# Optimization experiments

Measured on AMD Instinct MI355X. Metric: run time of the kernel, lower is better.

## Reference

```python
import jax, jax.numpy as jnp
import numpy as np

D_MODEL = 1024
NUM_HEADS = 16
HEAD_SIZE = D_MODEL // NUM_HEADS
ROPE_BASE = 10000.0
RMS_EPS = 1e-6


def rms_norm(x, scale):
    # torchtune RMSNorm: fp32 compute, eps=1e-6, learned scale
    xf = x.astype(jnp.float32)
    n = xf * jax.lax.rsqrt(jnp.mean(xf * xf, axis=-1, keepdims=True) + RMS_EPS)
    return (n * scale).astype(x.dtype)


def rope(x):
    # torchtune RotaryPositionalEmbeddings: interleaved pairs. x: [B,T,H,hd]
    B, T, H, hd = x.shape
    half = hd // 2
    theta = 1.0 / (ROPE_BASE ** (jnp.arange(0, hd, 2, dtype=jnp.float32) / hd))  # [half]
    ang = jnp.arange(T, dtype=jnp.float32)[:, None] * theta[None, :]  # [T,half]
    cos = jnp.cos(ang)[None, :, None, :]  # [1,T,1,half]
    sin = jnp.sin(ang)[None, :, None, :]
    xs = x.reshape(B, T, H, half, 2)
    x0, x1 = xs[..., 0], xs[..., 1]
    out = jnp.stack([x0 * cos - x1 * sin, x1 * cos + x0 * sin], axis=-1)
    return out.reshape(B, T, H, hd).astype(x.dtype)


def setup_inputs() -> dict:
    key = jax.random.key(0)
    ks = jax.random.split(key, 10)
    s = 0.02
    D = D_MODEL
    return {
        "x": jax.random.normal(ks[0], (2, 2048, D), dtype=jnp.float32),
        "rms_scale": jnp.ones((D,), dtype=jnp.float32),
        "in_proj_w": jax.random.normal(ks[1], (3 * D, D), dtype=jnp.float32) * s,
        "in_proj_b": jnp.zeros((3 * D,), dtype=jnp.float32),
        "out_proj_w": jax.random.normal(ks[2], (D, D), dtype=jnp.float32) * s,
        "out_proj_b": jnp.zeros((D,), dtype=jnp.float32),
        "w1": jax.random.normal(ks[3], (4 * D, D), dtype=jnp.float32) * s,
        "b1": jnp.zeros((4 * D,), dtype=jnp.float32),
        "w2": jax.random.normal(ks[4], (D, 4 * D), dtype=jnp.float32) * s,
        "b2": jnp.zeros((D,), dtype=jnp.float32),
    }


def reference(x, rms_scale, in_proj_w, in_proj_b, out_proj_w, out_proj_b, w1, b1, w2, b2):
    B, T, D = x.shape
    H, hd = NUM_HEADS, HEAD_SIZE

    xn = rms_norm(x, rms_scale)
    # RoPE on pre-projection q/k (as in original module), value = xn
    q_in = rope(xn.reshape(B, T, H, hd)).reshape(B, T, D)
    k_in = rope(xn.reshape(B, T, H, hd)).reshape(B, T, D)
    v_in = xn

    Wq, Wk, Wv = jnp.split(in_proj_w, 3, axis=0)
    bq, bk, bv = jnp.split(in_proj_b, 3, axis=0)
    q = (q_in @ Wq.T + bq).reshape(B, T, H, hd).transpose(0, 2, 1, 3)  # [B,H,T,hd]
    k = (k_in @ Wk.T + bk).reshape(B, T, H, hd).transpose(0, 2, 1, 3)
    v = (v_in @ Wv.T + bv).reshape(B, T, H, hd).transpose(0, 2, 1, 3)

    scores = jnp.einsum('bhqd,bhkd->bhqk', q, k) / jnp.sqrt(jnp.float32(hd))
    causal = jnp.tril(jnp.ones((T, T), dtype=bool))  # True = keep
    scores = jnp.where(causal[None, None], scores, jnp.float32(-1e30))
    attn = jax.nn.softmax(scores, axis=-1)
    ctx = jnp.einsum('bhqk,bhkd->bhqd', attn, v)  # [B,H,T,hd]
    attn_out = ctx.transpose(0, 2, 1, 3).reshape(B, T, D) @ out_proj_w.T + out_proj_b

    # NOTE: original overwrites x with attention output (no residual on attention)
    y = attn_out
    yn = rms_norm(y, rms_scale)
    ffn = jax.nn.silu(yn @ w1.T + b1) @ w2.T + b2
    return y + ffn
```

## Files before the change

kernel.cpp:

```cpp
#include <hip/hip_runtime.h>
#include <math.h>
#include <stdint.h>

#define D_MODEL 1024
#define NUM_HEADS 16
#define HEAD_SIZE 64
#define SEQ_T 2048

typedef __bf16 bf16;
typedef __bf16 bf16x8 __attribute__((ext_vector_type(8)));
typedef float f32x4 __attribute__((ext_vector_type(4)));

__device__ __forceinline__ void gld_lds16(const bf16* g, bf16* l) {
    __builtin_amdgcn_global_load_lds(
        (__attribute__((address_space(1))) void*)(const_cast<bf16*>(g)),
        (__attribute__((address_space(3))) void*)(l), 16, 0, 0);
}

struct __align__(8) b4pack { bf16 v[4]; };

__global__ __launch_bounds__(256) void cast_all_weights(const float* __restrict__ s0, bf16* __restrict__ d0, int n0,
                                                        const float* __restrict__ s1, bf16* __restrict__ d1, int n1,
                                                        const float* __restrict__ s2, bf16* __restrict__ d2, int n2,
                                                        const float* __restrict__ s3, bf16* __restrict__ d3, int n3) {
    int i = (blockIdx.x * 256 + threadIdx.x) * 4;
    const float* src;
    bf16* dst;
    if (i < n0) { src = s0; dst = d0; }
    else if (i < n0 + n1) { i -= n0; src = s1; dst = d1; }
    else if (i < n0 + n1 + n2) { i -= n0 + n1; src = s2; dst = d2; }
    else { i -= n0 + n1 + n2; if (i >= n3) return; src = s3; dst = d3; }
    float4 v = *(const float4*)(src + i);
    b4pack o;
    o.v[0] = (bf16)v.x; o.v[1] = (bf16)v.y; o.v[2] = (bf16)v.z; o.v[3] = (bf16)v.w;
    *(b4pack*)(dst + i) = o;
}

__global__ __launch_bounds__(256) void rmsnorm_rope_kernel(const float* __restrict__ x,
                                                           const float* __restrict__ scale,
                                                           bf16* __restrict__ xn,
                                                           bf16* __restrict__ rp, int T) {
    __shared__ float red[4];
    int row = blockIdx.x;
    int t = row % T;
    const float* xp = x + (size_t)row * D_MODEL;
    int tid = threadIdx.x;
    float4 xv = *(const float4*)(xp + tid * 4);
    float s = xv.x * xv.x + xv.y * xv.y + xv.z * xv.z + xv.w * xv.w;
    for (int off = 32; off; off >>= 1) s += __shfl_down(s, off);
    if ((tid & 63) == 0) red[tid >> 6] = s;
    __syncthreads();
    if (tid == 0) red[0] = red[0] + red[1] + red[2] + red[3];
    __syncthreads();
    float inv = rsqrtf(red[0] * (1.0f / D_MODEL) + 1e-6f);
    float4 sc = *(const float4*)(scale + tid * 4);
    float n0 = xv.x * inv * sc.x, n1 = xv.y * inv * sc.y;
    float n2 = xv.z * inv * sc.z, n3 = xv.w * inv * sc.w;
    b4pack pn;
    pn.v[0] = (bf16)n0; pn.v[1] = (bf16)n1; pn.v[2] = (bf16)n2; pn.v[3] = (bf16)n3;
    *(b4pack*)(xn + (size_t)row * D_MODEL + tid * 4) = pn;
    int p0 = 2 * tid;
    float th0 = expf(-0.2878231366242557f * (float)(p0 & 31));
    float th1 = expf(-0.2878231366242557f * (float)((p0 + 1) & 31));
    float s0, c0, s1, c1;
    sincosf((float)t * th0, &s0, &c0);
    sincosf((float)t * th1, &s1, &c1);
    b4pack pr;
    pr.v[0] = (bf16)(n0 * c0 - n1 * s0);
    pr.v[1] = (bf16)(n1 * c0 + n0 * s0);
    pr.v[2] = (bf16)(n2 * c1 - n3 * s1);
    pr.v[3] = (bf16)(n3 * c1 + n2 * s1);
    *(b4pack*)(rp + (size_t)row * D_MODEL + tid * 4) = pr;
}

__global__ __launch_bounds__(256) void rmsnorm_kernel(const float* __restrict__ x,
                                                      const float* __restrict__ scale,
                                                      bf16* __restrict__ out) {
    __shared__ float red[4];
    int row = blockIdx.x;
    const float* xp = x + (size_t)row * D_MODEL;
    bf16* op = out + (size_t)row * D_MODEL;
    int tid = threadIdx.x;
    float s = 0.f;
    for (int i = tid; i < D_MODEL; i += 256) { float v = xp[i]; s += v * v; }
    for (int off = 32; off; off >>= 1) s += __shfl_down(s, off);
    if ((tid & 63) == 0) red[tid >> 6] = s;
    __syncthreads();
    if (tid == 0) red[0] = red[0] + red[1] + red[2] + red[3];
    __syncthreads();
    float inv = rsqrtf(red[0] * (1.0f / D_MODEL) + 1e-6f);
    for (int i = tid; i < D_MODEL; i += 256) op[i] = (bf16)(xp[i] * inv * scale[i]);
}

template <int ACT, int ADD, int OUT_BF16, int VT>
__global__ __launch_bounds__(256) void gemm_bf16(const bf16* __restrict__ A,
                                                 const bf16* __restrict__ A2, int splitN,
                                                 const bf16* __restrict__ W,
                                                 const float* __restrict__ bias,
                                                 float* __restrict__ Cf,
                                                 bf16* __restrict__ Cb,
                                                 bf16* __restrict__ Vtp, int Tlen,
                                                 int M, int N, int K) {
    __shared__ __align__(16) bf16 As[2][128 * 64];
    __shared__ __align__(16) bf16 Bs[2][128 * 64];
    int tid = threadIdx.x;
    int m0 = blockIdx.y * 128, n0 = blockIdx.x * 128;
    const bf16* Ag = (n0 < splitN) ? A : A2;

    int lane = tid & 63, w = tid >> 6;
    int wm = w >> 1, wn = w & 1;
    int lm = lane & 15, quad = lane >> 4;
    int lm7 = lm & 7;

    f32x4 acc[4][4];
#pragma unroll
    for (int i = 0; i < 4; i++)
#pragma unroll
        for (int j = 0; j < 4; j++)
#pragma unroll
            for (int r = 0; r < 4; r++) acc[i][j][r] = 0.f;

    int nt = K >> 6;

#pragma unroll
    for (int i = 0; i < 4; i++) {
        int cch = tid + 256 * i;
        int r = cch >> 3, cc = (cch & 7) ^ (r & 7);
        gld_lds16(Ag + (size_t)(m0 + r) * K + cc * 8, &As[0][0] + cch * 8);
        gld_lds16(W  + (size_t)(n0 + r) * K + cc * 8, &Bs[0][0] + cch * 8);
    }

    for (int t = 0; t < nt; ++t) {
        int cur = t & 1;
        if (t + 1 < nt) {
            int k0 = (t + 1) << 6;
            bf16* as = &As[cur ^ 1][0];
            bf16* bs = &Bs[cur ^ 1][0];
#pragma unroll
            for (int i = 0; i < 4; i++) {
                int cch = tid + 256 * i;
                int r = cch >> 3, cc = (cch & 7) ^ (r & 7);
                gld_lds16(Ag + (size_t)(m0 + r) * K + k0 + cc * 8, as + cch * 8);
                gld_lds16(W  + (size_t)(n0 + r) * K + k0 + cc * 8, bs + cch * 8);
            }
            asm volatile("s_waitcnt vmcnt(8)" ::: "memory");
        } else {
            asm volatile("s_waitcnt vmcnt(0)" ::: "memory");
        }
        __builtin_amdgcn_s_barrier();

        const bf16* as = &As[cur][0];
        const bf16* bs = &Bs[cur][0];
        bf16x8 af[4][2], bfr[4][2];
#pragma unroll
        for (int i = 0; i < 4; i++) {
            int row = wm * 64 + i * 16 + lm;
#pragma unroll
            for (int h2 = 0; h2 < 2; h2++)
                af[i][h2] = *(const bf16x8*)&as[row * 64 + ((h2 * 4 + quad) ^ lm7) * 8];
        }
#pragma unroll
        for (int j = 0; j < 4; j++) {
            int row = wn * 64 + j * 16 + lm;
#pragma unroll
            for (int h2 = 0; h2 < 2; h2++)
                bfr[j][h2] = *(const bf16x8*)&bs[row * 64 + ((h2 * 4 + quad) ^ lm7) * 8];
        }
#pragma unroll
        for (int i = 0; i < 4; i++)
#pragma unroll
            for (int j = 0; j < 4; j++) {
                acc[i][j] = __builtin_amdgcn_mfma_f32_16x16x32_bf16(af[i][0], bfr[j][0], acc[i][j], 0, 0, 0);
                acc[i][j] = __builtin_amdgcn_mfma_f32_16x16x32_bf16(af[i][1], bfr[j][1], acc[i][j], 0, 0, 0);
            }
        asm volatile("" ::: "memory");
        __builtin_amdgcn_s_barrier();
    }

    if (VT && n0 >= 2 * D_MODEL) {
#pragma unroll
        for (int j = 0; j < 4; j++) {
            int col = n0 + wn * 64 + j * 16 + lm;
            int dimg = col - 2 * D_MODEL;
            float bv = bias[col];
#pragma unroll
            for (int i = 0; i < 4; i++) {
                int row0 = m0 + wm * 64 + i * 16 + quad * 4;
                int bb = row0 / Tlen, t0 = row0 % Tlen;
                b4pack pk;
#pragma unroll
                for (int r = 0; r < 4; r++) pk.v[r] = (bf16)(acc[i][j][r] + bv);
                *(b4pack*)(Vtp + ((size_t)bb * D_MODEL + dimg) * Tlen + t0) = pk;
            }
        }
        return;
    }

#pragma unroll
    for (int j = 0; j < 4; j++) {
        int col = n0 + wn * 64 + j * 16 + lm;
        float bv = bias[col];
#pragma unroll
        for (int i = 0; i < 4; i++) {
#pragma unroll
            for (int r = 0; r < 4; r++) {
                int row = m0 + wm * 64 + i * 16 + quad * 4 + r;
                float v = acc[i][j][r] + bv;
                if (ACT == 1) v = v / (1.f + __expf(-v));
                size_t idx = (size_t)row * N + col;
                if (ADD) v += Cf[idx];
                if (OUT_BF16) Cb[idx] = (bf16)v;
                else Cf[idx] = v;
            }
        }
    }
}

template <int SPLIT>
__global__ __launch_bounds__(256) void gemm128_sk(const bf16* __restrict__ A,
                                                  const bf16* __restrict__ W,
                                                  const float* __restrict__ bias,
                                                  float* __restrict__ Cf,
                                                  int M, int N, int K) {
    __shared__ __align__(16) bf16 As[2][128 * 64];
    __shared__ __align__(16) bf16 Bs[2][128 * 64];
    int tid = threadIdx.x;

    int nblk = gridDim.x;
    int q = nblk >> 3;
    int swz = (blockIdx.x & 7) * q + (blockIdx.x >> 3);
    int nnb = N >> 7;
    int nb = swz % nnb;
    int rem = swz / nnb;
    int mblocks = M >> 7;
    int mb = rem % mblocks;
    int sp = rem / mblocks;
    int m0 = mb * 128, n0 = nb * 128;
    int kc = K / SPLIT;
    int kbeg = sp * kc;

    int lane = tid & 63, w = tid >> 6;
    int wm = w >> 1, wn = w & 1;
    int lm = lane & 15, quad = lane >> 4;
    int lm7 = lm & 7;

    f32x4 acc[4][4];
#pragma unroll
    for (int i = 0; i < 4; i++)
#pragma unroll
        for (int j = 0; j < 4; j++)
#pragma unroll
            for (int r = 0; r < 4; r++) acc[i][j][r] = 0.f;

    int nt = kc >> 6;

#pragma unroll
    for (int i = 0; i < 4; i++) {
        int cch = tid + 256 * i;
        int r = cch >> 3, cc = (cch & 7) ^ (r & 7);
        gld_lds16(A + (size_t)(m0 + r) * K + kbeg + cc * 8, &As[0][0] + cch * 8);
        gld_lds16(W + (size_t)(n0 + r) * K + kbeg + cc * 8, &Bs[0][0] + cch * 8);
    }

    for (int t = 0; t < nt; ++t) {
        int cur = t & 1;
        if (t + 1 < nt) {
            int k0 = kbeg + ((t + 1) << 6);
            bf16* as = &As[cur ^ 1][0];
            bf16* bs = &Bs[cur ^ 1][0];
#pragma unroll
            for (int i = 0; i < 4; i++) {
                int cch = tid + 256 * i;
                int r = cch >> 3, cc = (cch & 7) ^ (r & 7);
                gld_lds16(A + (size_t)(m0 + r) * K + k0 + cc * 8, as + cch * 8);
                gld_lds16(W + (size_t)(n0 + r) * K + k0 + cc * 8, bs + cch * 8);
            }
            asm volatile("s_waitcnt vmcnt(8)" ::: "memory");
        } else {
            asm volatile("s_waitcnt vmcnt(0)" ::: "memory");
        }
        __builtin_amdgcn_s_barrier();

        const bf16* as = &As[cur][0];
        const bf16* bs = &Bs[cur][0];
        bf16x8 af[4][2], bfr[4][2];
#pragma unroll
        for (int i = 0; i < 4; i++) {
            int row = wm * 64 + i * 16 + lm;
#pragma unroll
            for (int h2 = 0; h2 < 2; h2++)
                af[i][h2] = *(const bf16x8*)&as[row * 64 + ((h2 * 4 + quad) ^ lm7) * 8];
        }
#pragma unroll
        for (int j = 0; j < 4; j++) {
            int row = wn * 64 + j * 16 + lm;
#pragma unroll
            for (int h2 = 0; h2 < 2; h2++)
                bfr[j][h2] = *(const bf16x8*)&bs[row * 64 + ((h2 * 4 + quad) ^ lm7) * 8];
        }
#pragma unroll
        for (int i = 0; i < 4; i++)
#pragma unroll
            for (int j = 0; j < 4; j++) {
                acc[i][j] = __builtin_amdgcn_mfma_f32_16x16x32_bf16(af[i][0], bfr[j][0], acc[i][j], 0, 0, 0);
                acc[i][j] = __builtin_amdgcn_mfma_f32_16x16x32_bf16(af[i][1], bfr[j][1], acc[i][j], 0, 0, 0);
            }
        asm volatile("" ::: "memory");
        __builtin_amdgcn_s_barrier();
    }

#pragma unroll
    for (int j = 0; j < 4; j++) {
        int col = n0 + wn * 64 + j * 16 + lm;
        float bv = (sp == 0) ? bias[col] : 0.f;
#pragma unroll
        for (int i = 0; i < 4; i++) {
#pragma unroll
            for (int r = 0; r < 4; r++) {
                int row = m0 + wm * 64 + i * 16 + quad * 4 + r;
                unsafeAtomicAdd(Cf + (size_t)row * N + col, acc[i][j][r] + bv);
            }
        }
    }
}

template <int ADD>
__global__ __launch_bounds__(256) void gemm_bf16_skinny2(const bf16* __restrict__ A,
                                                         const bf16* __restrict__ W,
                                                         const float* __restrict__ bias,
                                                         float* __restrict__ Cf,
                                                         int M, int N, int K) {
    __shared__ __align__(16) bf16 As[2][64 * 64];
    __shared__ __align__(16) bf16 Bs[2][128 * 64];
    int tid = threadIdx.x;

    int nblk = gridDim.x;
    int q = nblk >> 3;
    int swz = (blockIdx.x & 7) * q + (blockIdx.x >> 3);
    int nb = swz & 7;
    int mb = swz >> 3;
    int m0 = mb * 64, n0 = nb * 128;

    int lane = tid & 63, w = tid >> 6;
    int wm = w >> 1, wn = w & 1;
    int lm = lane & 15, quad = lane >> 4;
    int lm7 = lm & 7;

    int ar0 = tid >> 3, ac0 = (tid & 7) ^ (ar0 & 7);
    int t1 = tid + 256;
    int ar1 = t1 >> 3, ac1 = (t1 & 7) ^ (ar1 & 7);

    f32x4 acc[2][4];
#pragma unroll
    for (int i = 0; i < 2; i++)
#pragma unroll
        for (int j = 0; j < 4; j++)
#pragma unroll
            for (int r = 0; r < 4; r++) acc[i][j][r] = 0.f;

    int nt = K >> 6;

    {
        gld_lds16(A + (size_t)(m0 + ar0) * K + ac0 * 8, &As[0][0] + tid * 8);
        gld_lds16(A + (size_t)(m0 + ar1) * K + ac1 * 8, &As[0][0] + t1 * 8);
#pragma unroll
        for (int i = 0; i < 4; i++) {
            int c = tid + 256 * i;
            int r = c >> 3, cc = (c & 7) ^ (r & 7);
            gld_lds16(W + (size_t)(n0 + r) * K + cc * 8, &Bs[0][0] + c * 8);
        }
    }

    for (int t = 0; t < nt; ++t) {
        int cur = t & 1;
        if (t + 1 < nt) {
            int k0 = (t + 1) << 6;
            bf16* as = &As[cur ^ 1][0];
            bf16* bs = &Bs[cur ^ 1][0];
            gld_lds16(A + (size_t)(m0 + ar0) * K + k0 + ac0 * 8, as + tid * 8);
            gld_lds16(A + (size_t)(m0 + ar1) * K + k0 + ac1 * 8, as + t1 * 8);
#pragma unroll
            for (int i = 0; i < 4; i++) {
                int c = tid + 256 * i;
                int r = c >> 3, cc = (c & 7) ^ (r & 7);
                gld_lds16(W + (size_t)(n0 + r) * K + k0 + cc * 8, bs + c * 8);
            }
            asm volatile("s_waitcnt vmcnt(6)" ::: "memory");
        } else {
            asm volatile("s_waitcnt vmcnt(0)" ::: "memory");
        }
        __builtin_amdgcn_s_barrier();

        const bf16* as = &As[cur][0];
        const bf16* bs = &Bs[cur][0];
        bf16x8 af[2][2], bfr[4][2];
#pragma unroll
        for (int i = 0; i < 2; i++) {
            int row = wm * 32 + i * 16 + lm;
#pragma unroll
            for (int h = 0; h < 2; h++)
                af[i][h] = *(const bf16x8*)&as[row * 64 + ((h * 4 + quad) ^ lm7) * 8];
        }
#pragma unroll
        for (int j = 0; j < 4; j++) {
            int row = wn * 64 + j * 16 + lm;
#pragma unroll
            for (int h = 0; h < 2; h++)
                bfr[j][h] = *(const bf16x8*)&bs[row * 64 + ((h * 4 + quad) ^ lm7) * 8];
        }
#pragma unroll
        for (int i = 0; i < 2; i++)
#pragma unroll
            for (int j = 0; j < 4; j++) {
                acc[i][j] = __builtin_amdgcn_mfma_f32_16x16x32_bf16(af[i][0], bfr[j][0], acc[i][j], 0, 0, 0);
                acc[i][j] = __builtin_amdgcn_mfma_f32_16x16x32_bf16(af[i][1], bfr[j][1], acc[i][j], 0, 0, 0);
            }
        asm volatile("" ::: "memory");
        __builtin_amdgcn_s_barrier();
    }

#pragma unroll
    for (int j = 0; j < 4; j++) {
        int col = n0 + wn * 64 + j * 16 + lm;
        float bv = bias[col];
#pragma unroll
        for (int i = 0; i < 2; i++) {
#pragma unroll
            for (int r = 0; r < 4; r++) {
                int row = m0 + wm * 32 + i * 16 + quad * 4 + r;
                float v = acc[i][j][r] + bv;
                size_t idx = (size_t)row * N + col;
                if (ADD) v += Cf[idx];
                Cf[idx] = v;
            }
        }
    }
}

__global__ __launch_bounds__(256, 2) void attn_mfma_kernel(const bf16* __restrict__ QKV,
                                                           const bf16* __restrict__ Vt,
                                                           bf16* __restrict__ Og, int T) {
    __shared__ __align__(16) bf16 Ks[2][2][64 * 64];
    __shared__ __align__(16) bf16 Vs[2][2][64 * 64];
    __shared__ __align__(16) bf16 Ps[4 * 16 * 64];
    const int ldq = 3 * D_MODEL;
    int bidx = blockIdx.x;
    int c = bidx & 7;
    int rest = bidx >> 3;
    int p = rest & 15;
    int bhoct = rest >> 4;
    int bh = bhoct * 8 + c;
    int qtA = 31 - p, qtB = p;
    int h = bh & (NUM_HEADS - 1), b = bh / NUM_HEADS;
    int tid = threadIdx.x;
    int w = tid >> 6, lane = tid & 63;
    int lm = lane & 15, quad = lane >> 4;
    int qrowA = qtA * 64 + w * 16, qrowB = qtB * 64 + w * 16;

    int s0 = tid, s1 = tid + 256;
    int sr0 = s0 >> 3, sc0 = (s0 & 7) ^ (sr0 & 7);
    int sr1 = s1 >> 3, sc1 = (s1 & 7) ^ (sr1 & 7);

    const bf16* QpA = QKV + ((size_t)(b * T + qrowA + lm)) * ldq + h * HEAD_SIZE + quad * 8;
    bf16x8 qfA0 = *(const bf16x8*)QpA;
    bf16x8 qfA1 = *(const bf16x8*)(QpA + 32);
    const bf16* QpB = QKV + ((size_t)(b * T + qrowB + lm)) * ldq + h * HEAD_SIZE + quad * 8;
    bf16x8 qfB0 = *(const bf16x8*)QpB;
    bf16x8 qfB1 = *(const bf16x8*)(QpB + 32);

    const bf16* Kbase = QKV + ((size_t)b * T) * ldq + D_MODEL + h * HEAD_SIZE;
    const bf16* Vbase = Vt + ((size_t)b * D_MODEL + h * HEAD_SIZE) * T;
    const float C = 0.1803368801111204f;
    bf16* PsW = Ps + w * 16 * 64;
    int lm7 = lm & 7;

    bf16x8 ones;
#pragma unroll
    for (int i = 0; i < 8; i++) ones[i] = (bf16)1.0f;

    f32x4 oA[4], oB[4], laccA, laccB;
#pragma unroll
    for (int r = 0; r < 4; r++) {
        oA[r] = (f32x4){0.f, 0.f, 0.f, 0.f};
        oB[r] = (f32x4){0.f, 0.f, 0.f, 0.f};
        laccA[r] = 0.f; laccB[r] = 0.f;
    }

    int nktA = (qtA + 2) >> 1;
    int nktB = (qtB + 2) >> 1;

    auto stage = [&](int buf, int k0) {
        gld_lds16(Kbase + (size_t)(k0 + sr0) * ldq + sc0 * 8, &Ks[buf][0][0] + s0 * 8);
        gld_lds16(Kbase + (size_t)(k0 + sr1) * ldq + sc1 * 8, &Ks[buf][0][0] + s1 * 8);
        gld_lds16(Kbase + (size_t)(k0 + 64 + sr0) * ldq + sc0 * 8, &Ks[buf][1][0] + s0 * 8);
        gld_lds16(Kbase + (size_t)(k0 + 64 + sr1) * ldq + sc1 * 8, &Ks[buf][1][0] + s1 * 8);
        gld_lds16(Vbase + (size_t)sr0 * T + k0 + sc0 * 8, &Vs[buf][0][0] + s0 * 8);
        gld_lds16(Vbase + (size_t)sr1 * T + k0 + sc1 * 8, &Vs[buf][0][0] + s1 * 8);
        gld_lds16(Vbase + (size_t)sr0 * T + k0 + 64 + sc0 * 8, &Vs[buf][1][0] + s0 * 8);
        gld_lds16(Vbase + (size_t)sr1 * T + k0 + 64 + sc1 * 8, &Vs[buf][1][0] + s1 * 8);
    };

    auto run_tile = [&](int cur, int k0, bf16x8 qf0, bf16x8 qf1, int qrow0,
                        f32x4 (&o)[4], f32x4& lacc, bool lastmask) {
        f32x4 sa[2][4];
        __builtin_amdgcn_s_setprio(1);
#pragma unroll
        for (int u = 0; u < 2; u++) {
            const bf16* Ksu = &Ks[cur][u][0];
#pragma unroll
            for (int jb = 0; jb < 4; jb++) {
                int n = jb * 16 + lm;
                bf16x8 kf0 = *(const bf16x8*)&Ksu[(n * 8 + (quad ^ lm7)) * 8];
                bf16x8 kf1 = *(const bf16x8*)&Ksu[(n * 8 + ((quad + 4) ^ lm7)) * 8];
                f32x4 a = {0.f, 0.f, 0.f, 0.f};
                a = __builtin_amdgcn_mfma_f32_16x16x32_bf16(qf0, kf0, a, 0, 0, 0);
                a = __builtin_amdgcn_mfma_f32_16x16x32_bf16(qf1, kf1, a, 0, 0, 0);
                sa[u][jb] = a;
            }
        }
        __builtin_amdgcn_s_setprio(0);
        if (lastmask) {
#pragma unroll
            for (int u = 0; u < 2; u++)
#pragma unroll
                for (int jb = 0; jb < 4; jb++)
#pragma unroll
                    for (int r = 0; r < 4; r++)
                        if (k0 + u * 64 + jb * 16 + lm > qrow0 + quad * 4 + r)
                            sa[u][jb][r] = -3.0e38f;
        }
#pragma unroll
        for (int u = 0; u < 2; u++) {
            const bf16* Vsu = &Vs[cur][u][0];
#pragma unroll
            for (int jb = 0; jb < 4; jb++) {
                int g = jb * 2 + (lm >> 3);
#pragma unroll
                for (int r = 0; r < 4; r++) {
                    int row = quad * 4 + r;
                    float pv = exp2f(sa[u][jb][r] * C);
                    PsW[row * 64 + ((g ^ (row & 7)) * 8) + lm7] = (bf16)pv;
                }
            }
            bf16x8 pf0 = *(const bf16x8*)&PsW[lm * 64 + ((quad ^ lm7) * 8)];
            bf16x8 pf1 = *(const bf16x8*)&PsW[lm * 64 + (((quad + 4) ^ lm7) * 8)];
            __builtin_amdgcn_s_setprio(1);
#pragma unroll
            for (int db = 0; db < 4; db++) {
                int n = db * 16 + lm;
                bf16x8 vf0 = *(const bf16x8*)&Vsu[(n * 8 + (quad ^ lm7)) * 8];
                bf16x8 vf1 = *(const bf16x8*)&Vsu[(n * 8 + ((quad + 4) ^ lm7)) * 8];
                o[db] = __builtin_amdgcn_mfma_f32_16x16x32_bf16(pf0, vf0, o[db], 0, 0, 0);
                o[db] = __builtin_amdgcn_mfma_f32_16x16x32_bf16(pf1, vf1, o[db], 0, 0, 0);
            }
            lacc = __builtin_amdgcn_mfma_f32_16x16x32_bf16(pf0, ones, lacc, 0, 0, 0);
            lacc = __builtin_amdgcn_mfma_f32_16x16x32_bf16(pf1, ones, lacc, 0, 0, 0);
            __builtin_amdgcn_s_setprio(0);
        }
    };

    stage(0, 0);
    for (int kt = 0; kt < nktA; kt++) {
        int cur = kt & 1;
        if (kt + 1 < nktA) {
            stage(cur ^ 1, (kt + 1) * 128);
            asm volatile("s_waitcnt vmcnt(8)" ::: "memory");
        } else {
            asm volatile("s_waitcnt vmcnt(0)" ::: "memory");
        }
        __builtin_amdgcn_s_barrier();
        asm volatile("" ::: "memory");
        int k0 = kt * 128;
        run_tile(cur, k0, qfA0, qfA1, qrowA, oA, laccA, kt == nktA - 1);
        if (kt < nktB)
            run_tile(cur, k0, qfB0, qfB1, qrowB, oB, laccB, kt == nktB - 1);
        asm volatile("" ::: "memory");
        __builtin_amdgcn_s_barrier();
    }

    {
        float inv[4];
#pragma unroll
        for (int r = 0; r < 4; r++) inv[r] = 1.f / laccA[r];
        bf16* Ob = Og + ((size_t)(b * T + qrowA + quad * 4)) * D_MODEL + h * HEAD_SIZE + lm;
#pragma unroll
        for (int r = 0; r < 4; r++)
#pragma unroll
            for (int db = 0; db < 4; db++)
                Ob[(size_t)r * D_MODEL + db * 16] = (bf16)(oA[db][r] * inv[r]);
    }
    {
        float inv[4];
#pragma unroll
        for (int r = 0; r < 4; r++) inv[r] = 1.f / laccB[r];
        bf16* Ob = Og + ((size_t)(b * T + qrowB + quad * 4)) * D_MODEL + h * HEAD_SIZE + lm;
#pragma unroll
        for (int r = 0; r < 4; r++)
#pragma unroll
            for (int db = 0; db < 4; db++)
                Ob[(size_t)r * D_MODEL + db * 16] = (bf16)(oB[db][r] * inv[r]);
    }
}

extern "C" void kernel_launch(void* const* d_in, const int* in_sizes, int n_in,
                              void* d_out, int out_size, void* d_ws, size_t ws_size,
                              hipStream_t stream) {
    const float* x          = (const float*)d_in[0];
    const float* rms_scale  = (const float*)d_in[1];
    const float* in_proj_w  = (const float*)d_in[2];
    const float* in_proj_b  = (const float*)d_in[3];
    const float* out_proj_w = (const float*)d_in[4];
    const float* out_proj_b = (const float*)d_in[5];
    const float* w1         = (const float*)d_in[6];
    const float* b1         = (const float*)d_in[7];
    const float* w2         = (const float*)d_in[8];
    const float* b2         = (const float*)d_in[9];
    float* out = (float*)d_out;

    const int rows = in_sizes[0] / D_MODEL;
    const int T = SEQ_T;
    const int B = rows / T;
    const int D = D_MODEL;

    bf16* inwb  = (bf16*)d_ws;
    bf16* outwb = inwb + (size_t)3 * D * D;
    bf16* w1b   = outwb + (size_t)D * D;
    bf16* w2b   = w1b + (size_t)4 * D * D;
    bf16* XNb   = w2b + (size_t)4 * D * D;
    bf16* RPb   = XNb + (size_t)rows * D;
    bf16* QKV   = RPb + (size_t)rows * D;
    bf16* Vt    = QKV + (size_t)rows * 3 * D;
    bf16* CTXb  = XNb;
    bf16* YNb   = RPb;
    bf16* H1b   = QKV;

    {
        int n0 = 3 * D * D, n1 = D * D, n2 = 4 * D * D, n3 = 4 * D * D;
        int tot4 = (n0 + n1 + n2 + n3) / 4;
        cast_all_weights<<<(tot4 + 255) / 256, 256, 0, stream>>>(
            in_proj_w, inwb, n0, out_proj_w, outwb, n1, w1, w1b, n2, w2, w2b, n3);
    }
    rmsnorm_rope_kernel<<<rows, 256, 0, stream>>>(x, rms_scale, XNb, RPb, T);
    {
        dim3 g(3 * D / 128, rows / 128);
        gemm_bf16<0, 0, 1, 1><<<g, 256, 0, stream>>>(RPb, XNb, 2 * D, inwb, in_proj_b,
                                                     nullptr, QKV, Vt, T, rows, 3 * D, D);
    }
    attn_mfma_kernel<<<B * NUM_HEADS * (T / 128), 256, 0, stream>>>(QKV, Vt, CTXb, T);
    {
        int nblk = (D / 128) * (rows / 64);
        gemm_bf16_skinny2<0><<<nblk, 256, 0, stream>>>(CTXb, outwb, out_proj_b, out,
                                                       rows, D, D);
    }
    rmsnorm_kernel<<<rows, 256, 0, stream>>>(out, rms_scale, YNb);
    {
        dim3 g(4 * D / 128, rows / 128);
        gemm_bf16<1, 0, 1, 0><<<g, 256, 0, stream>>>(YNb, YNb, 4 * D, w1b, b1,
                                                     nullptr, H1b, nullptr, 1, rows, 4 * D, D);
    }
    {
        int nblk = 2 * (rows / 128) * (D / 128);
        gemm128_sk<2><<<nblk, 256, 0, stream>>>(H1b, w2b, b2, out, rows, D, 4 * D);
    }
}
```

Baseline: 327.1 us.

## Use 256x256-tile 512-thread GEMM kernel for FFN up-projection

Adds a new gemm256 kernel with 256x256 output tiles, 8 waves, double-buffered LDS via direct global-to-LDS loads, XOR-swizzled layout and an XCD-aware block swizzle. It is used for the w1 GEMM with SiLU epilogue, replacing the 128x128 gemm_bf16. Larger tiles raise arithmetic intensity and reduce global/LDS traffic per FLOP. In exchange they bring higher register and LDS pressure (128KB LDS per block, 128 accumulators per thread) and only 256 blocks, which may limit occupancy.

```diff
diff --git a/kernel.cpp b/kernel.cpp
--- a/kernel.cpp
+++ b/kernel.cpp
@@ -216,6 +216,101 @@
     }
 }
 
+template <int ACT>
+__global__ __launch_bounds__(512, 2) void gemm256(const bf16* __restrict__ A,
+                                                  const bf16* __restrict__ W,
+                                                  const float* __restrict__ bias,
+                                                  bf16* __restrict__ Cb,
+                                                  int M, int N, int K) {
+    __shared__ __align__(16) bf16 As[2][256 * 64];
+    __shared__ __align__(16) bf16 Bs[2][256 * 64];
+    int tid = threadIdx.x;
+
+    int nblk = gridDim.x;
+    int q = nblk >> 3;
+    int swz = (blockIdx.x & 7) * q + (blockIdx.x >> 3);
+    int nnb = N >> 8;
+    int nb = swz % nnb, mb = swz / nnb;
+    int m0 = mb * 256, n0 = nb * 256;
+
+    int lane = tid & 63, wid = tid >> 6;
+    int wm = wid >> 2, wn = wid & 3;
+    int lm = lane & 15, quad = lane >> 4;
+    int lm7 = lm & 7;
+
+    f32x4 acc[8][4];
+#pragma unroll
+    for (int i = 0; i < 8; i++)
+#pragma unroll
+        for (int j = 0; j < 4; j++)
+#pragma unroll
+            for (int r = 0; r < 4; r++) acc[i][j][r] = 0.f;
+
+    int nt = K >> 6;
+
+    auto stage = [&](int buf, int k0) {
+#pragma unroll
+        for (int i = 0; i < 4; i++) {
+            int cch = tid + 512 * i;
+            int r = cch >> 3, cc = (cch & 7) ^ (r & 7);
+            gld_lds16(A + (size_t)(m0 + r) * K + k0 + cc * 8, &As[buf][0] + cch * 8);
+            gld_lds16(W + (size_t)(n0 + r) * K + k0 + cc * 8, &Bs[buf][0] + cch * 8);
+        }
+    };
+
+    stage(0, 0);
+    asm volatile("s_waitcnt vmcnt(0)" ::: "memory");
+    __builtin_amdgcn_s_barrier();
+
+    for (int t = 0; t < nt; ++t) {
+        int cur = t & 1;
+        if (t + 1 < nt) stage(cur ^ 1, (t + 1) << 6);
+
+        const bf16* as = &As[cur][0];
+        const bf16* bs = &Bs[cur][0];
+        bf16x8 bfr[4][2];
+#pragma unroll
+        for (int j = 0; j < 4; j++) {
+            int row = wn * 64 + j * 16 + lm;
+#pragma unroll
+            for (int h2 = 0; h2 < 2; h2++)
+                bfr[j][h2] = *(const bf16x8*)&bs[row * 64 + ((h2 * 4 + quad) ^ lm7) * 8];
+        }
+#pragma unroll
+        for (int i = 0; i < 8; i++) {
+            int row = wm * 128 + i * 16 + lm;
+            bf16x8 af0 = *(const bf16x8*)&as[row * 64 + ((quad) ^ lm7) * 8];
+            bf16x8 af1 = *(const bf16x8*)&as[row * 64 + ((4 + quad) ^ lm7) * 8];
+            __builtin_amdgcn_s_setprio(1);
+#pragma unroll
+            for (int j = 0; j < 4; j++) {
+                acc[i][j] = __builtin_amdgcn_mfma_f32_16x16x32_bf16(af0, bfr[j][0], acc[i][j], 0, 0, 0);
+                acc[i][j] = __builtin_amdgcn_mfma_f32_16x16x32_bf16(af1, bfr[j][1], acc[i][j], 0, 0, 0);
+            }
+            __builtin_amdgcn_s_setprio(0);
+        }
+        asm volatile("s_waitcnt vmcnt(0)" ::: "memory");
+        asm volatile("" ::: "memory");
+        __builtin_amdgcn_s_barrier();
+    }
+
+#pragma unroll
+    for (int j = 0; j < 4; j++) {
+        int col = n0 + wn * 64 + j * 16 + lm;
+        float bv = bias[col];
+#pragma unroll
+        for (int i = 0; i < 8; i++) {
+#pragma unroll
+            for (int r = 0; r < 4; r++) {
+                int row = m0 + wm * 128 + i * 16 + quad * 4 + r;
+                float v = acc[i][j][r] + bv;
+                if (ACT == 1) v = v / (1.f + __expf(-v));
+                Cb[(size_t)row * N + col] = (bf16)v;
+            }
+        }
+    }
+}
+
 template <int SPLIT>
 __global__ __launch_bounds__(256) void gemm128_sk(const bf16* __restrict__ A,
                                                   const bf16* __restrict__ W,
@@ -654,9 +749,8 @@
     }
     rmsnorm_kernel<<<rows, 256, 0, stream>>>(out, rms_scale, YNb);
     {
-        dim3 g(4 * D / 128, rows / 128);
-        gemm_bf16<1, 0, 1, 0><<<g, 256, 0, stream>>>(YNb, YNb, 4 * D, w1b, b1,
-                                                     nullptr, H1b, nullptr, 1, rows, 4 * D, D);
+        int nblk = (rows / 256) * (4 * D / 256);
+        gemm256<1><<<nblk, 512, 0, stream>>>(YNb, w1b, b1, H1b, rows, 4 * D, D);
     }
     {
         int nblk = 2 * (rows / 128) * (D / 128);
```

New measurement: 331.8 us. No clear change (+1.4%).

## Use 256x128 triple-buffered GEMM with 512 threads for both FFN matmuls

Applied to the files above, without the earlier changes.

Replaces the split-K FFN2 kernel and the generic FFN1 GEMM with one templated kernel that uses 256x128 output tiles, 8 waves per block, and a three-stage LDS ring so loads run two K-steps ahead. It also raises wave priority around the MFMA loop. The aim is more reuse of each loaded weight tile and better hiding of memory latency. In exchange LDS use per block grows to about 144KB, which limits how many blocks fit on a CU, and the grid has fewer blocks.

```diff
diff --git a/kernel.cpp b/kernel.cpp
--- a/kernel.cpp
+++ b/kernel.cpp
@@ -216,14 +216,15 @@
     }
 }
 
-template <int SPLIT>
-__global__ __launch_bounds__(256) void gemm128_sk(const bf16* __restrict__ A,
-                                                  const bf16* __restrict__ W,
-                                                  const float* __restrict__ bias,
-                                                  float* __restrict__ Cf,
-                                                  int M, int N, int K) {
-    __shared__ __align__(16) bf16 As[2][128 * 64];
-    __shared__ __align__(16) bf16 Bs[2][128 * 64];
+template <int ACT, int SPLIT, int OUT_BF16>
+__global__ __launch_bounds__(512, 2) void gemm_ffn(const bf16* __restrict__ A,
+                                                   const bf16* __restrict__ W,
+                                                   const float* __restrict__ bias,
+                                                   float* __restrict__ Cf,
+                                                   bf16* __restrict__ Cb,
+                                                   int M, int N, int K) {
+    __shared__ __align__(16) bf16 As[3][256 * 64];
+    __shared__ __align__(16) bf16 Bs[3][128 * 64];
     int tid = threadIdx.x;
 
     int nblk = gridDim.x;
@@ -232,15 +233,15 @@
     int nnb = N >> 7;
     int nb = swz % nnb;
     int rem = swz / nnb;
-    int mblocks = M >> 7;
+    int mblocks = M >> 8;
     int mb = rem % mblocks;
     int sp = rem / mblocks;
-    int m0 = mb * 128, n0 = nb * 128;
+    int m0 = mb * 256, n0 = nb * 128;
     int kc = K / SPLIT;
     int kbeg = sp * kc;
 
-    int lane = tid & 63, w = tid >> 6;
-    int wm = w >> 1, wn = w & 1;
+    int lane = tid & 63, wid = tid >> 6;
+    int wm = wid >> 1, wn = wid & 1;
     int lm = lane & 15, quad = lane >> 4;
     int lm7 = lm & 7;
 
@@ -254,35 +255,38 @@
 
     int nt = kc >> 6;
 
-#pragma unroll
-    for (int i = 0; i < 4; i++) {
-        int cch = tid + 256 * i;
-        int r = cch >> 3, cc = (cch & 7) ^ (r & 7);
-        gld_lds16(A + (size_t)(m0 + r) * K + kbeg + cc * 8, &As[0][0] + cch * 8);
-        gld_lds16(W + (size_t)(n0 + r) * K + kbeg + cc * 8, &Bs[0][0] + cch * 8);
-    }
-
+    auto stage = [&](int buf, int k0) {
+#pragma unroll
+        for (int i = 0; i < 4; i++) {
+            int cch = tid + 512 * i;
+            int r = cch >> 3, cc = (cch & 7) ^ (r & 7);
+            gld_lds16(A + (size_t)(m0 + r) * K + k0 + cc * 8, &As[buf][0] + cch * 8);
+        }
+#pragma unroll
+        for (int i = 0; i < 2; i++) {
+            int cch = tid + 512 * i;
+            int r = cch >> 3, cc = (cch & 7) ^ (r & 7);
+            gld_lds16(W + (size_t)(n0 + r) * K + k0 + cc * 8, &Bs[buf][0] + cch * 8);
+        }
+    };
+
+    stage(0, kbeg);
+    if (nt > 1) stage(1, kbeg + 64);
+
+    int b0 = 0, b1 = 1, b2 = 2;
     for (int t = 0; t < nt; ++t) {
-        int cur = t & 1;
-        if (t + 1 < nt) {
-            int k0 = kbeg + ((t + 1) << 6);
-            bf16* as = &As[cur ^ 1][0];
-            bf16* bs = &Bs[cur ^ 1][0];
-#pragma unroll
-            for (int i = 0; i < 4; i++) {
-                int cch = tid + 256 * i;
-                int r = cch >> 3, cc = (cch & 7) ^ (r & 7);
-                gld_lds16(A + (size_t)(m0 + r) * K + k0 + cc * 8, as + cch * 8);
-                gld_lds16(W + (size_t)(n0 + r) * K + k0 + cc * 8, bs + cch * 8);
-            }
-            asm volatile("s_waitcnt vmcnt(8)" ::: "memory");
+        if (t + 2 < nt) {
+            stage(b2, kbeg + ((t + 2) << 6));
+            asm volatile("s_waitcnt vmcnt(12)" ::: "memory");
+        } else if (t + 1 < nt) {
+            asm volatile("s_waitcnt vmcnt(6)" ::: "memory");
         } else {
             asm volatile("s_waitcnt vmcnt(0)" ::: "memory");
         }
         __builtin_amdgcn_s_barrier();
 
-        const bf16* as = &As[cur][0];
-        const bf16* bs = &Bs[cur][0];
+        const bf16* as = &As[b0][0];
+        const bf16* bs = &Bs[b0][0];
         bf16x8 af[4][2], bfr[4][2];
 #pragma unroll
         for (int i = 0; i < 4; i++) {
@@ -298,6 +302,7 @@
             for (int h2 = 0; h2 < 2; h2++)
                 bfr[j][h2] = *(const bf16x8*)&bs[row * 64 + ((h2 * 4 + quad) ^ lm7) * 8];
         }
+        __builtin_amdgcn_s_setprio(1);
 #pragma unroll
         for (int i = 0; i < 4; i++)
 #pragma unroll
@@ -305,20 +310,25 @@
                 acc[i][j] = __builtin_amdgcn_mfma_f32_16x16x32_bf16(af[i][0], bfr[j][0], acc[i][j], 0, 0, 0);
                 acc[i][j] = __builtin_amdgcn_mfma_f32_16x16x32_bf16(af[i][1], bfr[j][1], acc[i][j], 0, 0, 0);
             }
+        __builtin_amdgcn_s_setprio(0);
         asm volatile("" ::: "memory");
         __builtin_amdgcn_s_barrier();
+        int tmp = b0; b0 = b1; b1 = b2; b2 = tmp;
     }
 
 #pragma unroll
     for (int j = 0; j < 4; j++) {
         int col = n0 + wn * 64 + j * 16 + lm;
-        float bv = (sp == 0) ? bias[col] : 0.f;
+        float bv = (SPLIT == 1 || sp == 0) ? bias[col] : 0.f;
 #pragma unroll
         for (int i = 0; i < 4; i++) {
 #pragma unroll
             for (int r = 0; r < 4; r++) {
                 int row = m0 + wm * 64 + i * 16 + quad * 4 + r;
-                unsafeAtomicAdd(Cf + (size_t)row * N + col, acc[i][j][r] + bv);
+                float v = acc[i][j][r] + bv;
+                if (ACT == 1) v = v / (1.f + __expf(-v));
+                if (OUT_BF16) Cb[(size_t)row * N + col] = (bf16)v;
+                else unsafeAtomicAdd(Cf + (size_t)row * N + col, v);
             }
         }
     }
@@ -654,12 +664,13 @@
     }
     rmsnorm_kernel<<<rows, 256, 0, stream>>>(out, rms_scale, YNb);
     {
-        dim3 g(4 * D / 128, rows / 128);
-        gemm_bf16<1, 0, 1, 0><<<g, 256, 0, stream>>>(YNb, YNb, 4 * D, w1b, b1,
-                                                     nullptr, H1b, nullptr, 1, rows, 4 * D, D);
-    }
-    {
-        int nblk = 2 * (rows / 128) * (D / 128);
-        gemm128_sk<2><<<nblk, 256, 0, stream>>>(H1b, w2b, b2, out, rows, D, 4 * D);
-    }
-}
+        int nblk = (rows / 256) * (4 * D / 128);
+        gemm_ffn<1, 1, 1><<<nblk, 512, 0, stream>>>(YNb, w1b, b1, nullptr, H1b,
+                                                    rows, 4 * D, D);
+    }
+    {
+        int nblk = 2 * (rows / 256) * (D / 128);
+        gemm_ffn<0, 2, 0><<<nblk, 512, 0, stream>>>(H1b, w2b, b2, out, nullptr,
+                                                    rows, D, 4 * D);
+    }
+}
```

Result: slower. 349.9 us (+7.0%).
